# Performance work log

Measured on AMD Instinct MI355X. Metric: run time of the kernel, lower is better.

The kernel has to match this reference:

```python
import jax, jax.numpy as jnp
import numpy as np

B, K, D, H, ZDIM = 65536, 16, 64, 128, 16

def setup_inputs() -> dict:
    key = jax.random.key(0)
    ks = jax.random.split(key, 20)
    s = 0.05
    inp = {
        'z': jax.random.normal(ks[0], (B, ZDIM), dtype=jnp.float32),
        'y': jax.random.randint(ks[1], (B,), 0, K),
        # backbone: 4 fc blocks (Linear+ReLU)
        'bw0': jax.random.normal(ks[2], (ZDIM, H), dtype=jnp.float32) * s,
        'bb0': jnp.zeros((H,), dtype=jnp.float32),
        'bw1': jax.random.normal(ks[3], (H, H), dtype=jnp.float32) * s,
        'bb1': jnp.zeros((H,), dtype=jnp.float32),
        'bw2': jax.random.normal(ks[4], (H, H), dtype=jnp.float32) * s,
        'bb2': jnp.zeros((H,), dtype=jnp.float32),
        'bw3': jax.random.normal(ks[5], (H, H), dtype=jnp.float32) * s,
        'bb3': jnp.zeros((H,), dtype=jnp.float32),
        # K heads, weights stacked on leading expert axis; layers 0-2 have ReLU, layer 3 does not
        'hw0': jax.random.normal(ks[6], (K, H, H), dtype=jnp.float32) * s,
        'hb0': jnp.zeros((K, H), dtype=jnp.float32),
        'hw1': jax.random.normal(ks[7], (K, H, H), dtype=jnp.float32) * s,
        'hb1': jnp.zeros((K, H), dtype=jnp.float32),
        'hw2': jax.random.normal(ks[8], (K, H, H), dtype=jnp.float32) * s,
        'hb2': jnp.zeros((K, H), dtype=jnp.float32),
        'hw3': jax.random.normal(ks[9], (K, H, D), dtype=jnp.float32) * s,
        'hb3': jnp.zeros((K, D), dtype=jnp.float32),
    }
    return inp

def reference(z, y, bw0, bb0, bw1, bb1, bw2, bb2, bw3, bb3,
              hw0, hb0, hw1, hb1, hw2, hb2, hw3, hb3):
    h = jax.nn.relu(z @ bw0 + bb0)
    h = jax.nn.relu(h @ bw1 + bb1)
    h = jax.nn.relu(h @ bw2 + bb2)
    h = jax.nn.relu(h @ bw3 + bb3)          # [B, H]
    # all K expert heads (faithful to original: compute all, then gather)
    a = jax.nn.relu(jnp.einsum('bi,kij->bkj', h, hw0) + hb0)  # [B, K, H]
    a = jax.nn.relu(jnp.einsum('bki,kij->bkj', a, hw1) + hb1)
    a = jax.nn.relu(jnp.einsum('bki,kij->bkj', a, hw2) + hb2)
    a = jnp.einsum('bki,kij->bkj', a, hw3) + hb3              # [B, K, D], no ReLU
    # select the y-th head per sample
    out = jnp.take_along_axis(a, y[:, None, None], axis=1)[:, 0, :]  # [B, D]
    return out
```

## Files before the change

### kernel.cpp

```cpp
#include <hip/hip_runtime.h>
#include <hip/hip_bf16.h>
#include <stdint.h>


typedef _Float16 f16;
typedef __attribute__((ext_vector_type(2)))  _Float16 f16x2;
typedef __attribute__((ext_vector_type(8)))  _Float16 f16x8;
typedef __attribute__((ext_vector_type(16))) float    f32x16;
typedef uint32_t u32;
typedef __attribute__((ext_vector_type(2))) u32 u32x2;
typedef __attribute__((ext_vector_type(4))) u32 u32x4;

#define MFMA(a, b, c) __builtin_amdgcn_mfma_f32_32x32x16_f16((a), (b), (c), 0, 0, 0)

constexpr int Bc = 65536;
constexpr int Kc = 16;
constexpr int Hc = 128;
constexpr int Dc = 64;

constexpr int CAP  = 4608;
constexpr int SPB  = 128;
constexpr int BPE  = CAP / SPB;
constexpr int NBLK = Kc * BPE;
constexpr int NXCD = 8;
constexpr int CHUNK = NBLK / NXCD;

constexpr int BBW_F16 = 2048 + 3 * 16384;
constexpr int HWE_F16 = 3 * 16384 + 8192;

constexpr int PREP_BLKS = 52 + Kc * 56;

struct Act { f16x8 w[8]; };

__device__ __forceinline__ f32x16 zero16() {
    f32x16 z;
#pragma unroll
    for (int i = 0; i < 16; ++i) z[i] = 0.0f;
    return z;
}

__device__ __forceinline__ void gload16(const f16* g, f16* l) {
    __builtin_amdgcn_global_load_lds(
        (const __attribute__((address_space(1))) void*)g,
        (__attribute__((address_space(3))) void*)l, 16, 0, 0);
}

__device__ __forceinline__ void stage_h(f16* dst, const f16* gW,
                                        int wid, int lane) {
#pragma unroll
    for (int i = 0; i < 4; ++i) {
        const int seg = wid * 4 + i;
        gload16(gW + seg * 512 + lane * 8, dst + seg * 512);
    }
}

template<bool RELU>
__device__ __forceinline__ void build_windows(
    const f32x16& c, const float4* bq, f16x8& w0, f16x8& w1)
{
    u32 P[8];
#pragma unroll
    for (int g = 0; g < 4; ++g) {
        const float bb[4] = {bq[g].x, bq[g].y, bq[g].z, bq[g].w};
        f16 h[4];
#pragma unroll
        for (int j = 0; j < 4; ++j) {
            float v = c[4 * g + j] + bb[j];
            if (RELU) v = fmaxf(v, 0.0f);
            h[j] = (f16)v;
        }
        f16x2 p0; p0[0] = h[0]; p0[1] = h[1];
        f16x2 p1; p1[0] = h[2]; p1[1] = h[3];
        P[2 * g]     = __builtin_bit_cast(u32, p0);
        P[2 * g + 1] = __builtin_bit_cast(u32, p1);
    }
    const u32x2 r02 = __builtin_amdgcn_permlane32_swap(P[0], P[2], false, false);
    const u32x2 r13 = __builtin_amdgcn_permlane32_swap(P[1], P[3], false, false);
    const u32x2 r46 = __builtin_amdgcn_permlane32_swap(P[4], P[6], false, false);
    const u32x2 r57 = __builtin_amdgcn_permlane32_swap(P[5], P[7], false, false);
    u32x4 W0 = { r02[0], r13[0], r02[1], r13[1] };
    u32x4 W1 = { r46[0], r57[0], r46[1], r57[1] };
    w0 = __builtin_bit_cast(f16x8, W0);
    w1 = __builtin_bit_cast(f16x8, W1);
}

template<bool STAGE_NEXT>
__device__ __forceinline__ void layer_half(
    f16* lds, int& par, const Act& src, Act& dst,
    const f16* gW, const f16* gWN,
    const float* __restrict__ biasG, int wid, int lane, int bh)
{
#pragma unroll
    for (int h = 0; h < 2; ++h) {
        if (h == 0)
            stage_h(lds + (par ^ 1) * 8192, gW + 8192, wid, lane);
        else if (STAGE_NEXT)
            stage_h(lds + (par ^ 1) * 8192, gWN, wid, lane);

#pragma unroll
        for (int qq = 0; qq < 2; ++qq) {
            const int q = 2 * h + qq;
            float4 bq[4];
#pragma unroll
            for (int g = 0; g < 4; ++g)
                bq[g] = *(const float4*)(biasG + 32 * q + 8 * g + 4 * bh);

            const f16* pw = lds + par * 8192 + qq * 4096 + lane * 8;
            f32x16 c0 = zero16(), c1 = zero16();
            __builtin_amdgcn_s_setprio(1);
#pragma unroll
            for (int ks = 0; ks < 8; ++ks) {
                const f16x8 wh = *(const f16x8*)(pw + ks * 512);
                if (ks & 1) c1 = MFMA(wh, src.w[ks], c1);
                else        c0 = MFMA(wh, src.w[ks], c0);
            }
            __builtin_amdgcn_s_setprio(0);
            const f32x16 cs = c0 + c1;
            build_windows<true>(cs, bq, dst.w[2 * q], dst.w[2 * q + 1]);
        }
        __syncthreads();
        par ^= 1;
    }
}

__device__ __forceinline__ void layer_final(
    const f16* lds, int par, const Act& src,
    const float* __restrict__ biasG,
    float* __restrict__ out, int bidx, int lane, int bh)
{
#pragma unroll
    for (int q = 0; q < 2; ++q) {
        float4 bq[4];
#pragma unroll
        for (int g = 0; g < 4; ++g)
            bq[g] = *(const float4*)(biasG + 32 * q + 8 * g + 4 * bh);

        const f16* pw = lds + par * 8192 + q * 4096 + lane * 8;
        f32x16 c0 = zero16(), c1 = zero16();
        __builtin_amdgcn_s_setprio(1);
#pragma unroll
        for (int ks = 0; ks < 8; ++ks) {
            const f16x8 wh = *(const f16x8*)(pw + ks * 512);
            if (ks & 1) c1 = MFMA(wh, src.w[ks], c1);
            else        c0 = MFMA(wh, src.w[ks], c0);
        }
        __builtin_amdgcn_s_setprio(0);
        if (bidx >= 0) {
            const f32x16 cs = c0 + c1;
#pragma unroll
            for (int g = 0; g < 4; ++g) {
                float4 v;
                v.x = cs[4 * g + 0] + bq[g].x;
                v.y = cs[4 * g + 1] + bq[g].y;
                v.z = cs[4 * g + 2] + bq[g].z;
                v.w = cs[4 * g + 3] + bq[g].w;
                *(float4*)(out + (size_t)bidx * Dc + 32 * q + 8 * g + 4 * bh) = v;
            }
        }
    }
}

__global__ __launch_bounds__(256, 3) void fused_mlp(
    const float* __restrict__ z,
    const int* __restrict__ idxb, const int* __restrict__ cursor,
    const f16* __restrict__ bbW,
    const float* __restrict__ bb0, const float* __restrict__ bb1,
    const float* __restrict__ bb2, const float* __restrict__ bb3,
    const f16* __restrict__ hW,
    const float* __restrict__ hb0, const float* __restrict__ hb1,
    const float* __restrict__ hb2, const float* __restrict__ hb3,
    float* __restrict__ out)
{
    __shared__ __attribute__((aligned(16))) f16 WLDS[2 * 8192];

    const int blk = (blockIdx.x % NXCD) * CHUNK + blockIdx.x / NXCD;
    const int e = blk / BPE;
    const int local0 = (blk % BPE) * SPB;
    const int cnt = min(cursor[e * 16], CAP);
    if (cnt - local0 <= 0) return;

    const int tid = threadIdx.x;
    const int wid = tid >> 6, lane = tid & 63;
    const int l31 = lane & 31, bh = lane >> 5;

    int bidx = -1;
    const int sIdx = local0 + wid * 32 + l31;
    if (sIdx < cnt) bidx = idxb[e * CAP + sIdx];

    f16x8 zw;
    if (bidx >= 0) {
        const float4 u0 = *(const float4*)(z + (size_t)bidx * 16 + bh * 8);
        const float4 u1 = *(const float4*)(z + (size_t)bidx * 16 + bh * 8 + 4);
        zw[0] = (f16)u0.x; zw[1] = (f16)u0.y; zw[2] = (f16)u0.z; zw[3] = (f16)u0.w;
        zw[4] = (f16)u1.x; zw[5] = (f16)u1.y; zw[6] = (f16)u1.z; zw[7] = (f16)u1.w;
    } else {
#pragma unroll
        for (int j = 0; j < 8; ++j) zw[j] = (f16)0.0f;
    }

    stage_h(WLDS, bbW + 2048, wid, lane);

    Act aA, aB;
#pragma unroll
    for (int q = 0; q < 4; ++q) {
        float4 bq[4];
#pragma unroll
        for (int g = 0; g < 4; ++g)
            bq[g] = *(const float4*)(bb0 + 32 * q + 8 * g + 4 * bh);
        const f16x8 wh = *(const f16x8*)(bbW + q * 512 + lane * 8);
        f32x16 c0 = zero16();
        c0 = MFMA(wh, zw, c0);
        build_windows<true>(c0, bq, aA.w[2 * q], aA.w[2 * q + 1]);
    }
    __syncthreads();
    int par = 0;

    const size_t we = (size_t)e * HWE_F16;
    layer_half<true>(WLDS, par, aA, aB, bbW + 2048,  bbW + 18432, bb1, wid, lane, bh);
    layer_half<true>(WLDS, par, aB, aA, bbW + 18432, bbW + 34816, bb2, wid, lane, bh);
    layer_half<true>(WLDS, par, aA, aB, bbW + 34816, hW + we,     bb3, wid, lane, bh);
    layer_half<true>(WLDS, par, aB, aA, hW + we,         hW + we + 16384,
                     hb0 + e * Hc, wid, lane, bh);
    layer_half<true>(WLDS, par, aA, aB, hW + we + 16384, hW + we + 32768,
                     hb1 + e * Hc, wid, lane, bh);
    layer_half<true>(WLDS, par, aB, aA, hW + we + 32768, hW + we + 49152,
                     hb2 + e * Hc, wid, lane, bh);
    layer_final(WLDS, par, aA, hb3 + e * Dc, out, bidx, lane, bh);
}

__global__ void prep_scatter(
    const float* __restrict__ bw0, const float* __restrict__ bw1,
    const float* __restrict__ bw2, const float* __restrict__ bw3,
    const float* __restrict__ hw0, const float* __restrict__ hw1,
    const float* __restrict__ hw2, const float* __restrict__ hw3,
    f16* __restrict__ bbW, f16* __restrict__ hW,
    const int* __restrict__ y, int* __restrict__ idxb, int* __restrict__ cursor)
{
    __shared__ float T[32][33];
    __shared__ int lc[Kc];
    __shared__ int lbase[Kc];
    const int id = blockIdx.x;
    const int tx = threadIdx.x;

    if (id >= PREP_BLKS) {
        if (tx < Kc) lc[tx] = 0;
        __syncthreads();
        const int b = (id - PREP_BLKS) * 256 + tx;
        const int e = y[b];
        const int r = atomicAdd(&lc[e], 1);
        __syncthreads();
        if (tx < Kc) lbase[tx] = atomicAdd(&cursor[tx * 16], lc[tx]);
        __syncthreads();
        const int slot = lbase[e] + r;
        if (slot < CAP) idxb[e * CAP + slot] = b;
        return;
    }

    const float* src; f16 *dh;
    int K, N, k0, n0;
    bool big;

    if (id < 52) {
        if (id < 4) {
            src = bw0; dh = bbW;
            K = 16; N = 128; k0 = 0; n0 = id * 32; big = false;
        } else {
            const int t = id - 4;
            const int l = t / 16, tile = t % 16;
            const float* bws[3] = {bw1, bw2, bw3};
            src = bws[l];
            dh = bbW + 2048 + l * 16384;
            K = 128; N = 128; big = true;
            k0 = (tile >> 2) * 32; n0 = (tile & 3) * 32;
        }
    } else {
        const int t = id - 52;
        const int e = t / 56, r = t % 56;
        if (r < 48) {
            const int l = r / 16, tile = r % 16;
            const float* hws[3] = {hw0, hw1, hw2};
            src = hws[l] + (size_t)e * 16384;
            dh = hW + (size_t)e * HWE_F16 + l * 16384;
            K = 128; N = 128; big = true;
            k0 = (tile >> 2) * 32; n0 = (tile & 3) * 32;
        } else {
            const int r2 = r - 48;
            src = hw3 + (size_t)e * 8192;
            dh = hW + (size_t)e * HWE_F16 + 49152;
            K = 128; N = 64; big = true;
            k0 = (r2 >> 1) * 32; n0 = (r2 & 1) * 32;
        }
    }

    const int c = tx & 31, g = tx >> 5;
#pragma unroll
    for (int i = 0; i < 4; ++i) {
        const int row = g * 4 + i;
        if (k0 + row < K)
            T[c][row] = src[(size_t)(k0 + row) * N + n0 + c];
    }
    __syncthreads();
#pragma unroll
    for (int i = 0; i < 4; ++i) {
        const int n = n0 + g * 4 + i;
        const int k = k0 + c;
        if (k < K) {
            const float v = T[g * 4 + i][c];
            size_t didx;
            if (big)
                didx = (size_t)(n >> 5) * 4096 + (size_t)(k >> 4) * 512
                     + ((k >> 3) & 1) * 256 + (n & 31) * 8 + (k & 7);
            else
                didx = (size_t)(n >> 5) * 512 + (size_t)(k >> 3) * 256
                     + (n & 31) * 8 + (k & 7);
            dh[didx] = (f16)v;
        }
    }
}

extern "C" void kernel_launch(void* const* d_in, const int* in_sizes, int n_in,
                              void* d_out, int out_size, void* d_ws, size_t ws_size,
                              hipStream_t stream)
{
    const float* z   = (const float*)d_in[0];
    const int*   y   = (const int*)d_in[1];
    const float* bw0 = (const float*)d_in[2];
    const float* bb0 = (const float*)d_in[3];
    const float* bw1 = (const float*)d_in[4];
    const float* bb1 = (const float*)d_in[5];
    const float* bw2 = (const float*)d_in[6];
    const float* bb2 = (const float*)d_in[7];
    const float* bw3 = (const float*)d_in[8];
    const float* bb3 = (const float*)d_in[9];
    const float* hw0 = (const float*)d_in[10];
    const float* hb0 = (const float*)d_in[11];
    const float* hw1 = (const float*)d_in[12];
    const float* hb1 = (const float*)d_in[13];
    const float* hw2 = (const float*)d_in[14];
    const float* hb2 = (const float*)d_in[15];
    const float* hw3 = (const float*)d_in[16];
    const float* hb3 = (const float*)d_in[17];
    float* out = (float*)d_out;

    char* p = (char*)d_ws;
    f16* bbW = (f16*)p;  p += (size_t)BBW_F16 * 2;
    f16* hW  = (f16*)p;  p += (size_t)Kc * HWE_F16 * 2;
    int* idxb = (int*)p; p += (size_t)Kc * CAP * 4;
    int* cursor = (int*)p;

    hipMemsetAsync(cursor, 0, 256 * sizeof(int), stream);

    prep_scatter<<<PREP_BLKS + Bc / 256, 256, 0, stream>>>(
        bw0, bw1, bw2, bw3, hw0, hw1, hw2, hw3,
        bbW, hW, y, idxb, cursor);

    fused_mlp<<<NBLK, 256, 0, stream>>>(
        z, idxb, cursor, bbW, bb0, bb1, bb2, bb3,
        hW, hb0, hb1, hb2, hb3, out);
}
```

Baseline: 132.9 us.

## Drop LDS weight staging; single-wave blocks read MFMA weights from global/L2

Removes the double-buffered LDS staging of weights via global_load_lds and the block-wide barriers. Each block becomes one 64-lane wave handling 32 samples, and it loads weight fragments straight from global memory, relying on L1/L2 caching. This drops synchronisation and LDS traffic and raises the block count fourfold. In exchange, every wave refetches the full weight set from cache, so weight bandwidth per sample rises and load latency is exposed directly before the MFMAs.

```diff
diff --git a/kernel.cpp b/kernel.cpp
--- a/kernel.cpp
+++ b/kernel.cpp
@@ -19,7 +19,7 @@
 constexpr int Dc = 64;
 
 constexpr int CAP  = 4608;
-constexpr int SPB  = 128;
+constexpr int SPB  = 32;
 constexpr int BPE  = CAP / SPB;
 constexpr int NBLK = Kc * BPE;
 constexpr int NXCD = 8;
@@ -37,21 +37,6 @@
 #pragma unroll
     for (int i = 0; i < 16; ++i) z[i] = 0.0f;
     return z;
-}
-
-__device__ __forceinline__ void gload16(const f16* g, f16* l) {
-    __builtin_amdgcn_global_load_lds(
-        (const __attribute__((address_space(1))) void*)g,
-        (__attribute__((address_space(3))) void*)l, 16, 0, 0);
-}
-
-__device__ __forceinline__ void stage_h(f16* dst, const f16* gW,
-                                        int wid, int lane) {
-#pragma unroll
-    for (int i = 0; i < 4; ++i) {
-        const int seg = wid * 4 + i;
-        gload16(gW + seg * 512 + lane * 8, dst + seg * 512);
-    }
 }
 
 template<bool RELU>
@@ -84,58 +69,44 @@
     w1 = __builtin_bit_cast(f16x8, W1);
 }
 
-template<bool STAGE_NEXT>
-__device__ __forceinline__ void layer_half(
-    f16* lds, int& par, const Act& src, Act& dst,
-    const f16* gW, const f16* gWN,
-    const float* __restrict__ biasG, int wid, int lane, int bh)
-{
-#pragma unroll
-    for (int h = 0; h < 2; ++h) {
-        if (h == 0)
-            stage_h(lds + (par ^ 1) * 8192, gW + 8192, wid, lane);
-        else if (STAGE_NEXT)
-            stage_h(lds + (par ^ 1) * 8192, gWN, wid, lane);
-
-#pragma unroll
-        for (int qq = 0; qq < 2; ++qq) {
-            const int q = 2 * h + qq;
-            float4 bq[4];
-#pragma unroll
-            for (int g = 0; g < 4; ++g)
-                bq[g] = *(const float4*)(biasG + 32 * q + 8 * g + 4 * bh);
-
-            const f16* pw = lds + par * 8192 + qq * 4096 + lane * 8;
-            f32x16 c0 = zero16(), c1 = zero16();
-            __builtin_amdgcn_s_setprio(1);
-#pragma unroll
-            for (int ks = 0; ks < 8; ++ks) {
-                const f16x8 wh = *(const f16x8*)(pw + ks * 512);
-                if (ks & 1) c1 = MFMA(wh, src.w[ks], c1);
-                else        c0 = MFMA(wh, src.w[ks], c0);
-            }
-            __builtin_amdgcn_s_setprio(0);
-            const f32x16 cs = c0 + c1;
-            build_windows<true>(cs, bq, dst.w[2 * q], dst.w[2 * q + 1]);
-        }
-        __syncthreads();
-        par ^= 1;
-    }
-}
-
-__device__ __forceinline__ void layer_final(
-    const f16* lds, int par, const Act& src,
-    const float* __restrict__ biasG,
-    float* __restrict__ out, int bidx, int lane, int bh)
-{
-#pragma unroll
-    for (int q = 0; q < 2; ++q) {
+__device__ __forceinline__ void layer_glb(
+    const f16* __restrict__ gW, const float* __restrict__ biasG,
+    const Act& src, Act& dst, int lane, int bh)
+{
+#pragma unroll
+    for (int q = 0; q < 4; ++q) {
+        const f16* pw = gW + q * 4096 + lane * 8;
         float4 bq[4];
 #pragma unroll
         for (int g = 0; g < 4; ++g)
             bq[g] = *(const float4*)(biasG + 32 * q + 8 * g + 4 * bh);
 
-        const f16* pw = lds + par * 8192 + q * 4096 + lane * 8;
+        f32x16 c0 = zero16(), c1 = zero16();
+        __builtin_amdgcn_s_setprio(1);
+#pragma unroll
+        for (int ks = 0; ks < 8; ++ks) {
+            const f16x8 wh = *(const f16x8*)(pw + ks * 512);
+            if (ks & 1) c1 = MFMA(wh, src.w[ks], c1);
+            else        c0 = MFMA(wh, src.w[ks], c0);
+        }
+        __builtin_amdgcn_s_setprio(0);
+        const f32x16 cs = c0 + c1;
+        build_windows<true>(cs, bq, dst.w[2 * q], dst.w[2 * q + 1]);
+    }
+}
+
+__device__ __forceinline__ void layer_final(
+    const f16* __restrict__ gW, const float* __restrict__ biasG,
+    const Act& src, float* __restrict__ out, int bidx, int lane, int bh)
+{
+#pragma unroll
+    for (int q = 0; q < 2; ++q) {
+        const f16* pw = gW + q * 4096 + lane * 8;
+        float4 bq[4];
+#pragma unroll
+        for (int g = 0; g < 4; ++g)
+            bq[g] = *(const float4*)(biasG + 32 * q + 8 * g + 4 * bh);
+
         f32x16 c0 = zero16(), c1 = zero16();
         __builtin_amdgcn_s_setprio(1);
 #pragma unroll
@@ -160,7 +131,7 @@
     }
 }
 
-__global__ __launch_bounds__(256, 3) void fused_mlp(
+__global__ __launch_bounds__(64, 2) void fused_mlp(
     const float* __restrict__ z,
     const int* __restrict__ idxb, const int* __restrict__ cursor,
     const f16* __restrict__ bbW,
@@ -171,20 +142,17 @@
     const float* __restrict__ hb2, const float* __restrict__ hb3,
     float* __restrict__ out)
 {
-    __shared__ __attribute__((aligned(16))) f16 WLDS[2 * 8192];
-
     const int blk = (blockIdx.x % NXCD) * CHUNK + blockIdx.x / NXCD;
     const int e = blk / BPE;
     const int local0 = (blk % BPE) * SPB;
     const int cnt = min(cursor[e * 16], CAP);
     if (cnt - local0 <= 0) return;
 
-    const int tid = threadIdx.x;
-    const int wid = tid >> 6, lane = tid & 63;
+    const int lane = threadIdx.x & 63;
     const int l31 = lane & 31, bh = lane >> 5;
 
     int bidx = -1;
-    const int sIdx = local0 + wid * 32 + l31;
+    const int sIdx = local0 + l31;
     if (sIdx < cnt) bidx = idxb[e * CAP + sIdx];
 
     f16x8 zw;
@@ -198,8 +166,6 @@
         for (int j = 0; j < 8; ++j) zw[j] = (f16)0.0f;
     }
 
-    stage_h(WLDS, bbW + 2048, wid, lane);
-
     Act aA, aB;
 #pragma unroll
     for (int q = 0; q < 4; ++q) {
@@ -212,20 +178,15 @@
         c0 = MFMA(wh, zw, c0);
         build_windows<true>(c0, bq, aA.w[2 * q], aA.w[2 * q + 1]);
     }
-    __syncthreads();
-    int par = 0;
 
     const size_t we = (size_t)e * HWE_F16;
-    layer_half<true>(WLDS, par, aA, aB, bbW + 2048,  bbW + 18432, bb1, wid, lane, bh);
-    layer_half<true>(WLDS, par, aB, aA, bbW + 18432, bbW + 34816, bb2, wid, lane, bh);
-    layer_half<true>(WLDS, par, aA, aB, bbW + 34816, hW + we,     bb3, wid, lane, bh);
-    layer_half<true>(WLDS, par, aB, aA, hW + we,         hW + we + 16384,
-                     hb0 + e * Hc, wid, lane, bh);
-    layer_half<true>(WLDS, par, aA, aB, hW + we + 16384, hW + we + 32768,
-                     hb1 + e * Hc, wid, lane, bh);
-    layer_half<true>(WLDS, par, aB, aA, hW + we + 32768, hW + we + 49152,
-                     hb2 + e * Hc, wid, lane, bh);
-    layer_final(WLDS, par, aA, hb3 + e * Dc, out, bidx, lane, bh);
+    layer_glb(bbW + 2048,      bb1,          aA, aB, lane, bh);
+    layer_glb(bbW + 18432,     bb2,          aB, aA, lane, bh);
+    layer_glb(bbW + 34816,     bb3,          aA, aB, lane, bh);
+    layer_glb(hW + we,         hb0 + e * Hc, aB, aA, lane, bh);
+    layer_glb(hW + we + 16384, hb1 + e * Hc, aA, aB, lane, bh);
+    layer_glb(hW + we + 32768, hb2 + e * Hc, aB, aA, lane, bh);
+    layer_final(hW + we + 49152, hb3 + e * Dc, aA, out, bidx, lane, bh);
 }
 
 __global__ void prep_scatter(
@@ -354,7 +315,7 @@
         bw0, bw1, bw2, bw3, hw0, hw1, hw2, hw3,
         bbW, hW, y, idxb, cursor);
 
-    fused_mlp<<<NBLK, 256, 0, stream>>>(
+    fused_mlp<<<NBLK, 64, 0, stream>>>(
         z, idxb, cursor, bbW, bb0, bb1, bb2, bb3,
         hW, hb0, hb1, hb2, hb3, out);
 }
```

Result: slower. 138.5 us (+4.2%).
